# Optimization experiments

Measured on AMD Instinct MI355X. Metric: run time of the kernel, lower is better.

Reference implementation:

```python
import jax, jax.numpy as jnp
import numpy as np

# cfg constants (init_kwargs)
NMS_THRESH = 0.6
CONF_THRESH = 0.05
TOPN = 1000           # nms_thresh_topN: pre-NMS cap and post-NMS cap
NUM_CLASSES = 80
CLS_OFFSET = 4096.0   # > max image coord; class-aware NMS via coordinate offset


def setup_inputs() -> dict:
    key = jax.random.key(0)
    k0, k1, k2, k3 = jax.random.split(key, 4)
    B, H, W, C = 16, 128, 128, NUM_CLASSES
    N = H * W
    image_h, image_w = 1024, 1024
    # anchor-point pixel coordinates for this FPN level
    locations = jax.random.uniform(k0, (N, 2), dtype=jnp.float32) * 1024.0
    pred_cls = jax.random.normal(k1, (B, H, W, C), dtype=jnp.float32)
    # (l, t, r, b) distances are positive
    pred_boxes = jax.random.uniform(k2, (B, H, W, 4), dtype=jnp.float32) * 64.0
    pred_centerness = jax.random.normal(k3, (B, H, W), dtype=jnp.float32)
    return {"locations": locations, "pred_cls": pred_cls, "pred_boxes": pred_boxes,
            "pred_centerness": pred_centerness, "image_h": image_h, "image_w": image_w}


def _pairwise_iou(b):  # b: [K, 4] xyxy
    x1, y1, x2, y2 = b[:, 0], b[:, 1], b[:, 2], b[:, 3]
    area = jnp.maximum(x2 - x1, 0.0) * jnp.maximum(y2 - y1, 0.0)
    ix1 = jnp.maximum(x1[:, None], x1[None, :])
    iy1 = jnp.maximum(y1[:, None], y1[None, :])
    ix2 = jnp.minimum(x2[:, None], x2[None, :])
    iy2 = jnp.minimum(y2[:, None], y2[None, :])
    inter = jnp.maximum(ix2 - ix1, 0.0) * jnp.maximum(iy2 - iy1, 0.0)
    return inter / (area[:, None] + area[None, :] - inter + 1e-9)


def _nms_keep(iou, valid):
    # greedy NMS over score-descending candidates; iou: [B,K,K], valid: [B,K] bool
    K = iou.shape[-1]
    ar = jnp.arange(K)

    def body(i, keep):
        iou_i = jax.lax.dynamic_index_in_dim(iou, i, axis=1, keepdims=False)  # [B,K]
        keep_i = jnp.take(keep, i, axis=1)                                    # [B]
        sup = (iou_i > NMS_THRESH) & (ar[None, :] > i) & keep_i[:, None]
        return keep & ~sup

    return jax.lax.fori_loop(0, K, body, valid)


def reference(locations, pred_cls, pred_boxes, pred_centerness, image_h, image_w):
    B, H, W, C = pred_cls.shape
    N = H * W
    cls = jax.nn.sigmoid(pred_cls.reshape(B, N, C))
    ctr = jax.nn.sigmoid(pred_centerness.reshape(B, N))
    boxes = pred_boxes.reshape(B, N, 4)
    scores = cls * ctr[:, :, None]                    # [B,N,C]
    mask = cls > CONF_THRESH
    neg = jnp.asarray(-jnp.inf, scores.dtype)
    flat = jnp.where(mask, scores, neg).reshape(B, N * C)
    # pre-NMS top-K over masked (location, class) candidates; emulates
    # cls_mask_top_n = clamp(mask.sum(), max=topN) + topk in the torch code
    vals, idx = jax.lax.top_k(flat, TOPN)             # [B,K]
    valid = jnp.isfinite(vals)
    loc_i = idx // C                                  # location index
    lab = idx % C + 1                                 # 1-based class label
    pb = jnp.take_along_axis(boxes, loc_i[:, :, None], axis=1)   # [B,K,4] (l,t,r,b)
    locs = locations[loc_i]                                       # [B,K,2]
    x1 = jnp.clip(locs[..., 0] - pb[..., 0], 0.0, image_w - 1)
    y1 = jnp.clip(locs[..., 1] - pb[..., 1], 0.0, image_h - 1)
    x2 = jnp.clip(locs[..., 0] + pb[..., 2], 0.0, image_w - 1)
    y2 = jnp.clip(locs[..., 1] + pb[..., 3], 0.0, image_h - 1)
    det = jnp.stack([x1, y1, x2, y2], axis=-1)        # [B,K,4] xyxy, clipped
    score = jnp.where(valid, vals, 0.0)
    # sort by score descending for greedy NMS
    order = jnp.argsort(-score, axis=1)
    score = jnp.take_along_axis(score, order, axis=1)
    valid = jnp.take_along_axis(valid, order, axis=1)
    lab = jnp.take_along_axis(lab, order, axis=1)
    det = jnp.take_along_axis(det, order[:, :, None], axis=1)
    # per-class NMS via class-offset trick (boxes of different classes never overlap)
    iou = jax.vmap(_pairwise_iou)(det + lab.astype(det.dtype)[:, :, None] * CLS_OFFSET)
    keep = _nms_keep(iou, valid) & valid
    # final topN (nms_thresh_topN) is a no-op here: candidates <= TOPN already
    boxes_out = det * keep[:, :, None].astype(det.dtype)
    scores_out = jnp.where(keep, score, 0.0)
    labels_out = jnp.where(keep, lab, 0)
    return boxes_out, scores_out, labels_out
```

## Files before the change

kernel.cpp:

```cpp
#include <hip/hip_runtime.h>

#define B_    16
#define N_    16384
#define C_    80
#define NC_   (N_ * C_)
#define TOPN_ 1000
#define SEGCAP_ 4096
#define T0_   0.70f
#define T0KEY_ 0x3F333333u
#define RKEY_  0x3E800000u
#define NBIN_  4096

#define OFF_CNT    0u
#define ZERO_BYTES 8192u
#define OFF_CAND   8192u

__device__ __forceinline__ float sigm(float x) { return 1.0f / (1.0f + expf(-x)); }

__device__ __forceinline__ int binof(unsigned key) {
    int b = (int)((key - RKEY_) >> 12);
    return b > (NBIN_ - 1) ? (NBIN_ - 1) : b;
}
__device__ __forceinline__ unsigned key_lb(int b) {
    return RKEY_ + ((unsigned)b << 12);
}

__global__ __launch_bounds__(256, 4) void k_pass1(const float* __restrict__ cls,
                                                  const float* __restrict__ ctr,
                                                  unsigned* __restrict__ cntp,
                                                  unsigned long long* __restrict__ cand) {
    __shared__ float xh[64];
    __shared__ float sbv[64];
    __shared__ unsigned long long stage[512];
    __shared__ unsigned lcnt, gbase, lcw;
    const int blk = blockIdx.x, t = threadIdx.x;
    const int b = blk >> 8, k = blk & 255;
    const int shard = k & 7;
    if (t == 0) lcnt = 0;
    if (t < 64) {
        float sc = sigm(ctr[b * N_ + k * 64 + t]);
        sbv[t] = sc;
        float q = T0_ / sc;
        xh[t] = (q < 1.f) ? (logf(q / (1.f - q)) - 1e-3f) : 3.0e38f;
    }
    __syncthreads();
    const float4* p = (const float4*)(cls + (size_t)b * NC_ + (size_t)k * 5120);
    float4 v[5];
    #pragma unroll
    for (int i = 0; i < 5; ++i) v[i] = p[5 * t + i];
    const int r = t >> 2;
    const float thr = xh[r];
    float mx = v[0].x;
    #pragma unroll
    for (int i = 0; i < 5; ++i)
        mx = fmaxf(mx, fmaxf(fmaxf(v[i].x, v[i].y), fmaxf(v[i].z, v[i].w)));
    if (mx >= thr) {
        const float sb = sbv[r];
        #pragma unroll
        for (int i = 0; i < 5; ++i) {
            float xs[4] = {v[i].x, v[i].y, v[i].z, v[i].w};
            #pragma unroll
            for (int j = 0; j < 4; ++j) {
                if (xs[j] >= thr) {
                    float sapx = sb * __builtin_amdgcn_rcpf(1.f + __expf(-xs[j]));
                    if (sapx >= T0_ * 0.999f) {
                        float s = sigm(xs[j]);
                        unsigned key = __float_as_uint(s * sb);
                        if (key >= T0KEY_) {
                            unsigned pos = atomicAdd(&lcnt, 1u);
                            if (pos < 512u) {
                                unsigned e = (unsigned)(k * 5120 + (5 * t + i) * 4 + j);
                                stage[pos] = ((unsigned long long)key << 32) |
                                             (unsigned long long)(0xFFFFFFFFu - e);
                            }
                        }
                    }
                }
            }
        }
    }
    __syncthreads();
    if (t == 0) {
        unsigned lc = lcnt; if (lc > 512u) lc = 512u;
        gbase = atomicAdd(&cntp[b * 128 + shard * 16], lc);
        lcw = lc;
    }
    __syncthreads();
    unsigned long long* seg = cand + ((size_t)(b * 8 + shard) << 12);
    for (unsigned i = t; i < lcw; i += 256) {
        unsigned gp = gbase + i;
        if (gp < SEGCAP_) seg[gp] = stage[i];
    }
}

union TailSMem {
    struct {
        unsigned hbin[NBIN_];
        unsigned binBase[NBIN_];
        unsigned long long srt[2048];
        unsigned long long srt2[1024];
    } s;
    struct {
        float4 bxo[1024];
        unsigned short clsList[1024];
        unsigned clsStart[81];
        unsigned clsCur[81];
        unsigned short supIdx[1024 * 16];
        unsigned char nsup[1024];
    } c;
};

__global__ __launch_bounds__(1024) void k_tail(
        unsigned long long* __restrict__ cand, unsigned* __restrict__ cntp,
        const float* __restrict__ boxes, const float* __restrict__ locs,
        const int* __restrict__ ph, const int* __restrict__ pw,
        const float* __restrict__ cls, const float* __restrict__ ctr,
        float* __restrict__ out) {
    __shared__ TailSMem u;
    __shared__ unsigned csh[8];
    __shared__ unsigned Lsh;
    __shared__ unsigned long long keepw[16];
    __shared__ unsigned long long vmaskSh[16];
    const int b = blockIdx.x, t = threadIdx.x;

    if (t < 8) { unsigned cc = cntp[b * 128 + t * 16]; csh[t] = cc > SEGCAP_ ? SEGCAP_ : cc; }
    __syncthreads();
    unsigned tot = 0;
    #pragma unroll
    for (int s = 0; s < 8; ++s) tot += csh[s];
    if (tot < (unsigned)TOPN_) {
        const float4* p = (const float4*)(cls + (size_t)b * NC_);
        for (unsigned f = t; f < (unsigned)(NC_ / 4); f += 1024) {
            float4 v = p[f];
            unsigned nl = f / 20;
            float sb = sigm(ctr[b * N_ + nl]);
            float xs[4] = {v.x, v.y, v.z, v.w};
            #pragma unroll
            for (int j = 0; j < 4; ++j) {
                float s = sigm(xs[j]);
                if (s > 0.05f) {
                    unsigned key = __float_as_uint(s * sb);
                    if (key >= RKEY_ && key < T0KEY_) {
                        int sh = t & 7;
                        unsigned pos = atomicAdd(&cntp[b * 128 + sh * 16], 1u);
                        if (pos < SEGCAP_) {
                            unsigned e = 4u * f + (unsigned)j;
                            cand[((size_t)(b * 8 + sh) << 12) + pos] =
                                ((unsigned long long)key << 32) |
                                (unsigned long long)(0xFFFFFFFFu - e);
                        }
                    }
                }
            }
        }
        __syncthreads();
        if (t < 8) { unsigned cc = cntp[b * 128 + t * 16]; csh[t] = cc > SEGCAP_ ? SEGCAP_ : cc; }
        __syncthreads();
    }

    #pragma unroll
    for (int i = 0; i < 4; ++i) u.s.hbin[t + 1024 * i] = 0;
    u.s.srt[t] = 0ull; u.s.srt[t + 1024] = 0ull;
    u.s.srt2[t] = 0ull;
    __syncthreads();
    const unsigned long long* g = cand + ((size_t)b << 15);
    for (int s = 0; s < 8; ++s) {
        unsigned cc = csh[s];
        const unsigned long long* gs = g + ((size_t)s << 12);
        for (unsigned o = t; o < cc; o += 1024)
            atomicAdd(&u.s.hbin[binof((unsigned)(gs[o] >> 32))], 1u);
    }
    __syncthreads();
    if (t < 64) {
        const int l = t;
        unsigned cs = 0;
        for (int i = 0; i < 64; ++i) cs += u.s.hbin[64 * l + i];
        unsigned S = cs;
        #pragma unroll
        for (int off = 1; off < 64; off <<= 1) {
            unsigned y = __shfl_down(S, off, 64);
            if (l + off < 64) S += y;
        }
        unsigned acc = S - cs;
        int bc_l = NBIN_;
        for (int b2 = 63; b2 >= 0; --b2) {
            int bin = 64 * l + b2;
            u.s.binBase[bin] = acc;
            if (acc < (unsigned)TOPN_) bc_l = bin;
            acc += u.s.hbin[bin];
        }
        #pragma unroll
        for (int off = 1; off < 64; off <<= 1) {
            int y = __shfl_down(bc_l, off, 64);
            bc_l = bc_l < y ? bc_l : y;
        }
        if (l == 0) Lsh = key_lb(bc_l < NBIN_ ? bc_l : 0);
    }
    __syncthreads();
    const unsigned Lk = Lsh;
    for (int s = 0; s < 8; ++s) {
        unsigned cc = csh[s];
        const unsigned long long* gs = g + ((size_t)s << 12);
        for (unsigned o = t; o < cc; o += 1024) {
            unsigned long long comp = gs[o];
            unsigned key = (unsigned)(comp >> 32);
            if (key >= Lk) {
                unsigned slot = atomicAdd(&u.s.binBase[binof(key)], 1u);
                if (slot < 2048u) u.s.srt[slot] = comp;
            }
        }
    }
    __syncthreads();
    #pragma unroll
    for (int pp = 0; pp < 2; ++pp) {
        unsigned p = (unsigned)t + 1024u * pp;
        unsigned long long comp = u.s.srt[p];
        if (comp) {
            int bin = binof((unsigned)(comp >> 32));
            unsigned endq = u.s.binBase[bin];
            unsigned pop = u.s.hbin[bin];
            unsigned beg = endq - pop;
            unsigned end2 = endq > 2048u ? 2048u : endq;
            unsigned rank = 0;
            for (unsigned j = beg; j < end2; ++j) rank += (u.s.srt[j] > comp);
            unsigned pos = beg + rank;
            if (pos < 1024u) u.s.srt2[pos] = comp;
        }
    }
    __syncthreads();
    unsigned long long comp = u.s.srt2[t];
    unsigned key = (unsigned)(comp >> 32);
    float4 d = {0.f, 0.f, 0.f, 0.f}, doff = {0.f, 0.f, 0.f, 0.f};
    float sc = 0.f; int lb = 0;
    if (key) {
        unsigned idx = 0xFFFFFFFFu - (unsigned)comp;
        unsigned loc = idx / (unsigned)C_;
        unsigned cc2 = idx - loc * (unsigned)C_;
        lb = (int)cc2 + 1;
        float4 pb = ((const float4*)boxes)[(size_t)b * N_ + loc];
        float lx = locs[2 * loc], ly = locs[2 * loc + 1];
        float Wm1 = (float)(pw[0] - 1), Hm1 = (float)(ph[0] - 1);
        d.x = fminf(fmaxf(lx - pb.x, 0.f), Wm1);
        d.y = fminf(fmaxf(ly - pb.y, 0.f), Hm1);
        d.z = fminf(fmaxf(lx + pb.z, 0.f), Wm1);
        d.w = fminf(fmaxf(ly + pb.w, 0.f), Hm1);
        sc = __uint_as_float(key);
        float off = (float)lb * 4096.0f;
        doff.x = d.x + off; doff.y = d.y + off; doff.z = d.z + off; doff.w = d.w + off;
    }
    const bool valid = (key != 0u);
    {
        unsigned long long ball = __ballot(valid);
        if ((t & 63) == 0) vmaskSh[t >> 6] = ball;
    }
    __syncthreads();

    u.c.bxo[t] = doff;
    if (t < 81) u.c.clsStart[t] = 0;
    __syncthreads();
    if (lb > 0) atomicAdd(&u.c.clsStart[lb], 1u);
    __syncthreads();
    if (t < 64) {
        const int l = t;
        unsigned s0 = 0, s1 = 0;
        if (l < 40) { s0 = u.c.clsStart[2 * l + 1]; s1 = u.c.clsStart[2 * l + 2]; }
        unsigned p = s0 + s1;
        unsigned S = p;
        #pragma unroll
        for (int off = 1; off < 64; off <<= 1) {
            unsigned y = __shfl_up(S, off, 64);
            if (l >= off) S += y;
        }
        unsigned excl = S - p;
        if (l < 40) {
            u.c.clsStart[2 * l + 1] = excl;
            u.c.clsCur[2 * l + 1]   = excl;
            u.c.clsStart[2 * l + 2] = excl + s0;
            u.c.clsCur[2 * l + 2]   = excl + s0;
        }
    }
    __syncthreads();
    if (lb > 0) {
        unsigned pos = atomicAdd(&u.c.clsCur[lb], 1u);
        u.c.clsList[pos] = (unsigned short)t;
    }
    __syncthreads();
    unsigned nsup = 0;
    if (valid) {
        float4 A = doff;
        float aA = fmaxf(A.z - A.x, 0.f) * fmaxf(A.w - A.y, 0.f);
        unsigned beg = u.c.clsStart[lb], end = u.c.clsCur[lb];
        for (unsigned q = beg; q < end; ++q) {
            int j = (int)u.c.clsList[q];
            if (j < t) {
                float4 Bv = u.c.bxo[j];
                float aB = fmaxf(Bv.z - Bv.x, 0.f) * fmaxf(Bv.w - Bv.y, 0.f);
                float ix1 = fmaxf(A.x, Bv.x), iy1 = fmaxf(A.y, Bv.y);
                float ix2 = fminf(A.z, Bv.z), iy2 = fminf(A.w, Bv.w);
                float inter = fmaxf(ix2 - ix1, 0.f) * fmaxf(iy2 - iy1, 0.f);
                float iou = inter / (aA + aB - inter + 1e-9f);
                if (iou > 0.6f) {
                    if (nsup < 16u) u.c.supIdx[t * 16 + nsup] = (unsigned short)j;
                    ++nsup;
                }
            }
        }
        if (nsup > 16u) nsup = 16u;
    }
    u.c.nsup[t] = (unsigned char)nsup;
    __syncthreads();

    if (t < 64) {
        const int ii = t;
        for (int gg = 0; gg < 16; ++gg) {
            const int row = gg * 64 + ii;
            const unsigned base = (unsigned)(gg << 6);
            unsigned ns = u.c.nsup[row];
            unsigned long long diag = 0;
            bool supP = false;
            for (unsigned q = 0; q < ns; ++q) {
                unsigned j = (unsigned)u.c.supIdx[row * 16 + q];
                if (j < base) {
                    if ((keepw[j >> 6] >> (j & 63)) & 1ull) supP = true;
                } else {
                    diag |= 1ull << (j & 63);
                }
            }
            bool alive = (((vmaskSh[gg] >> ii) & 1ull) != 0) && !supP;
            unsigned long long undec = __ballot(alive);
            unsigned long long kept = 0;
            while (undec) {
                bool meU = ((undec >> ii) & 1ull) != 0;
                bool supK = (kept & diag) != 0;
                bool anyU = (undec & diag) != 0;
                unsigned long long bkm = __ballot(meU && !supK && !anyU);
                unsigned long long brm = __ballot(meU && supK);
                kept |= bkm;
                undec &= ~(bkm | brm);
            }
            if (ii == 0) keepw[gg] = kept;
        }
    }
    __syncthreads();

    if (t < TOPN_) {
        bool kp = ((keepw[t >> 6] >> (t & 63)) & 1ull) != 0;
        ((float4*)out)[(size_t)b * TOPN_ + t] = kp ? d : make_float4(0.f, 0.f, 0.f, 0.f);
        out[B_ * TOPN_ * 4 + b * TOPN_ + t] = kp ? sc : 0.f;
        out[B_ * TOPN_ * 5 + b * TOPN_ + t] = kp ? (float)lb : 0.f;
    }
}

extern "C" void kernel_launch(void* const* d_in, const int* in_sizes, int n_in,
                              void* d_out, int out_size, void* d_ws, size_t ws_size,
                              hipStream_t stream) {
    (void)in_sizes; (void)n_in; (void)out_size; (void)ws_size;
    const float* locations = (const float*)d_in[0];
    const float* pred_cls  = (const float*)d_in[1];
    const float* pred_box  = (const float*)d_in[2];
    const float* pred_ctr  = (const float*)d_in[3];
    const int*   ph        = (const int*)d_in[4];
    const int*   pw        = (const int*)d_in[5];
    float* out = (float*)d_out;

    char* w = (char*)d_ws;
    unsigned* cntp           = (unsigned*)(w + OFF_CNT);
    unsigned long long* cand = (unsigned long long*)(w + OFF_CAND);

    hipMemsetAsync(w, 0, ZERO_BYTES, stream);

    k_pass1<<<4096, 256, 0, stream>>>(pred_cls, pred_ctr, cntp, cand);
    k_tail<<<B_, 1024, 0, stream>>>(cand, cntp, pred_box, locations, ph, pw,
                                    pred_cls, pred_ctr, out);
}
```

Measured before the change: 164.9 us.

## Give each pass1 block a private candidate segment and drop the workspace memset

New measurement: 169.4 us. +2.8%, slower.

```diff
diff --git a/kernel.cpp b/kernel.cpp
--- a/kernel.cpp
+++ b/kernel.cpp
@@ -5,15 +5,16 @@
 #define C_    80
 #define NC_   (N_ * C_)
 #define TOPN_ 1000
-#define SEGCAP_ 4096
 #define T0_   0.70f
 #define T0KEY_ 0x3F333333u
 #define RKEY_  0x3E800000u
 #define NBIN_  4096
+#define BLKCAP_ 512
+#define RESCCAP_ 8192
 
 #define OFF_CNT    0u
-#define ZERO_BYTES 8192u
-#define OFF_CAND   8192u
+#define OFF_CAND   16384u
+#define OFF_RESC   (16384u + 16777216u)
 
 __device__ __forceinline__ float sigm(float x) { return 1.0f / (1.0f + expf(-x)); }
 
@@ -27,15 +28,14 @@
 
 __global__ __launch_bounds__(256, 4) void k_pass1(const float* __restrict__ cls,
                                                   const float* __restrict__ ctr,
-                                                  unsigned* __restrict__ cntp,
+                                                  unsigned* __restrict__ cnt,
                                                   unsigned long long* __restrict__ cand) {
     __shared__ float xh[64];
     __shared__ float sbv[64];
-    __shared__ unsigned long long stage[512];
-    __shared__ unsigned lcnt, gbase, lcw;
+    __shared__ unsigned long long stage[BLKCAP_];
+    __shared__ unsigned lcnt;
     const int blk = blockIdx.x, t = threadIdx.x;
     const int b = blk >> 8, k = blk & 255;
-    const int shard = k & 7;
     if (t == 0) lcnt = 0;
     if (t < 64) {
         float sc = sigm(ctr[b * N_ + k * 64 + t]);
@@ -68,7 +68,7 @@
                         unsigned key = __float_as_uint(s * sb);
                         if (key >= T0KEY_) {
                             unsigned pos = atomicAdd(&lcnt, 1u);
-                            if (pos < 512u) {
+                            if (pos < (unsigned)BLKCAP_) {
                                 unsigned e = (unsigned)(k * 5120 + (5 * t + i) * 4 + j);
                                 stage[pos] = ((unsigned long long)key << 32) |
                                              (unsigned long long)(0xFFFFFFFFu - e);
@@ -80,17 +80,10 @@
         }
     }
     __syncthreads();
-    if (t == 0) {
-        unsigned lc = lcnt; if (lc > 512u) lc = 512u;
-        gbase = atomicAdd(&cntp[b * 128 + shard * 16], lc);
-        lcw = lc;
-    }
-    __syncthreads();
-    unsigned long long* seg = cand + ((size_t)(b * 8 + shard) << 12);
-    for (unsigned i = t; i < lcw; i += 256) {
-        unsigned gp = gbase + i;
-        if (gp < SEGCAP_) seg[gp] = stage[i];
-    }
+    unsigned lc = lcnt; if (lc > (unsigned)BLKCAP_) lc = (unsigned)BLKCAP_;
+    if (t == 0) cnt[blk] = lc;
+    unsigned long long* seg = cand + ((size_t)blk << 9);
+    for (unsigned i = t; i < lc; i += 256) seg[i] = stage[i];
 }
 
 union TailSMem {
@@ -111,24 +104,35 @@
 };
 
 __global__ __launch_bounds__(1024) void k_tail(
-        unsigned long long* __restrict__ cand, unsigned* __restrict__ cntp,
+        const unsigned long long* __restrict__ cand, const unsigned* __restrict__ cnt,
+        unsigned long long* __restrict__ resc,
         const float* __restrict__ boxes, const float* __restrict__ locs,
         const int* __restrict__ ph, const int* __restrict__ pw,
         const float* __restrict__ cls, const float* __restrict__ ctr,
         float* __restrict__ out) {
     __shared__ TailSMem u;
-    __shared__ unsigned csh[8];
-    __shared__ unsigned Lsh;
+    __shared__ unsigned csh[256];
+    __shared__ unsigned Lsh, totSh, rcnt, rcwSh;
     __shared__ unsigned long long keepw[16];
     __shared__ unsigned long long vmaskSh[16];
     const int b = blockIdx.x, t = threadIdx.x;
-
-    if (t < 8) { unsigned cc = cntp[b * 128 + t * 16]; csh[t] = cc > SEGCAP_ ? SEGCAP_ : cc; }
-    __syncthreads();
-    unsigned tot = 0;
-    #pragma unroll
-    for (int s = 0; s < 8; ++s) tot += csh[s];
-    if (tot < (unsigned)TOPN_) {
+    const int wv = t >> 6, lane = t & 63;
+
+    if (t == 0) { rcnt = 0; rcwSh = 0; }
+    if (t < 256) {
+        unsigned cc = cnt[b * 256 + t];
+        csh[t] = cc > (unsigned)BLKCAP_ ? (unsigned)BLKCAP_ : cc;
+    }
+    __syncthreads();
+    if (t < 64) {
+        unsigned s4 = csh[4 * t] + csh[4 * t + 1] + csh[4 * t + 2] + csh[4 * t + 3];
+        #pragma unroll
+        for (int off = 32; off >= 1; off >>= 1) s4 += __shfl_down(s4, off, 64);
+        if (t == 0) totSh = s4;
+    }
+    __syncthreads();
+    if (totSh < (unsigned)TOPN_) {
+        unsigned long long* rs = resc + ((size_t)b << 13);
         const float4* p = (const float4*)(cls + (size_t)b * NC_);
         for (unsigned f = t; f < (unsigned)(NC_ / 4); f += 1024) {
             float4 v = p[f];
@@ -141,20 +145,21 @@
                 if (s > 0.05f) {
                     unsigned key = __float_as_uint(s * sb);
                     if (key >= RKEY_ && key < T0KEY_) {
-                        int sh = t & 7;
-                        unsigned pos = atomicAdd(&cntp[b * 128 + sh * 16], 1u);
-                        if (pos < SEGCAP_) {
+                        unsigned pos = atomicAdd(&rcnt, 1u);
+                        if (pos < (unsigned)RESCCAP_) {
                             unsigned e = 4u * f + (unsigned)j;
-                            cand[((size_t)(b * 8 + sh) << 12) + pos] =
-                                ((unsigned long long)key << 32) |
-                                (unsigned long long)(0xFFFFFFFFu - e);
+                            rs[pos] = ((unsigned long long)key << 32) |
+                                      (unsigned long long)(0xFFFFFFFFu - e);
                         }
                     }
                 }
             }
         }
         __syncthreads();
-        if (t < 8) { unsigned cc = cntp[b * 128 + t * 16]; csh[t] = cc > SEGCAP_ ? SEGCAP_ : cc; }
+        if (t == 0) {
+            unsigned rc = rcnt;
+            rcwSh = rc > (unsigned)RESCCAP_ ? (unsigned)RESCCAP_ : rc;
+        }
         __syncthreads();
     }
 
@@ -163,13 +168,18 @@
     u.s.srt[t] = 0ull; u.s.srt[t + 1024] = 0ull;
     u.s.srt2[t] = 0ull;
     __syncthreads();
-    const unsigned long long* g = cand + ((size_t)b << 15);
-    for (int s = 0; s < 8; ++s) {
+    const unsigned long long* g = cand + ((size_t)b << 17);
+    const unsigned long long* rs = resc + ((size_t)b << 13);
+    const unsigned rcw = rcwSh;
+    for (int si = 0; si < 16; ++si) {
+        int s = wv * 16 + si;
         unsigned cc = csh[s];
-        const unsigned long long* gs = g + ((size_t)s << 12);
-        for (unsigned o = t; o < cc; o += 1024)
+        const unsigned long long* gs = g + ((size_t)s << 9);
+        for (unsigned o = lane; o < cc; o += 64)
             atomicAdd(&u.s.hbin[binof((unsigned)(gs[o] >> 32))], 1u);
     }
+    for (unsigned o = t; o < rcw; o += 1024)
+        atomicAdd(&u.s.hbin[binof((unsigned)(rs[o] >> 32))], 1u);
     __syncthreads();
     if (t < 64) {
         const int l = t;
@@ -198,16 +208,25 @@
     }
     __syncthreads();
     const unsigned Lk = Lsh;
-    for (int s = 0; s < 8; ++s) {
+    for (int si = 0; si < 16; ++si) {
+        int s = wv * 16 + si;
         unsigned cc = csh[s];
-        const unsigned long long* gs = g + ((size_t)s << 12);
-        for (unsigned o = t; o < cc; o += 1024) {
+        const unsigned long long* gs = g + ((size_t)s << 9);
+        for (unsigned o = lane; o < cc; o += 64) {
             unsigned long long comp = gs[o];
             unsigned key = (unsigned)(comp >> 32);
             if (key >= Lk) {
                 unsigned slot = atomicAdd(&u.s.binBase[binof(key)], 1u);
                 if (slot < 2048u) u.s.srt[slot] = comp;
             }
+        }
+    }
+    for (unsigned o = t; o < rcw; o += 1024) {
+        unsigned long long comp = rs[o];
+        unsigned key = (unsigned)(comp >> 32);
+        if (key >= Lk) {
+            unsigned slot = atomicAdd(&u.s.binBase[binof(key)], 1u);
+            if (slot < 2048u) u.s.srt[slot] = comp;
         }
     }
     __syncthreads();
@@ -364,12 +383,12 @@
     float* out = (float*)d_out;
 
     char* w = (char*)d_ws;
-    unsigned* cntp           = (unsigned*)(w + OFF_CNT);
+    unsigned* cnt            = (unsigned*)(w + OFF_CNT);
     unsigned long long* cand = (unsigned long long*)(w + OFF_CAND);
-
-    hipMemsetAsync(w, 0, ZERO_BYTES, stream);
-
-    k_pass1<<<4096, 256, 0, stream>>>(pred_cls, pred_ctr, cntp, cand);
-    k_tail<<<B_, 1024, 0, stream>>>(cand, cntp, pred_box, locations, ph, pw,
+    unsigned long long* resc = (unsigned long long*)(w + OFF_RESC);
+
+
+    k_pass1<<<4096, 256, 0, stream>>>(pred_cls, pred_ctr, cnt, cand);
+    k_tail<<<B_, 1024, 0, stream>>>(cand, cnt, resc, pred_box, locations, ph, pw,
                                     pred_cls, pred_ctr, out);
 }
```
